# Optimization experiments

Hardware: AMD Instinct MI355X
Metric: run time of the kernel (lower is better)

The kernel has to match this reference:

```python
import jax, jax.numpy as jnp
import numpy as np

D = 1024      # in_dim
HS = 64       # head_size
H = 16        # num_heads
B, S = 2, 2048


def setup_inputs() -> dict:
    key = jax.random.key(0)
    k1, k2, k3, k4, k5, k6 = jax.random.split(key, 6)
    scale = 1.0 / np.sqrt(D)
    x = jax.random.normal(k1, (B, S, D), dtype=jnp.float32)
    # Stacked per-head projection weights (torch Linear weight is [out,in];
    # random init so layout only needs to be consistent). query weight exists
    # in the torch module but is never used (source bug), so it is omitted.
    Wk = jax.random.normal(k2, (H, D, HS), dtype=jnp.float32) * scale
    Wv = jax.random.normal(k3, (H, D, HS), dtype=jnp.float32) * scale
    Wproj = jax.random.normal(k4, (H * HS, D), dtype=jnp.float32) * (1.0 / np.sqrt(H * HS))
    bproj = jax.random.normal(k5, (D,), dtype=jnp.float32) * 0.01
    return {"x": x, "Wk": Wk, "Wv": Wv, "Wproj": Wproj, "bproj": bproj}


def reference(x, Wk, Wv, Wproj, bproj):
    # Faithful to source: k = key(x); q = value(x); v = value(x)  (q == v, no softmax)
    k = jnp.einsum("bsd,hde->bhse", x, Wk)   # [B,H,S,HS]
    v = jnp.einsum("bsd,hde->bhse", x, Wv)   # [B,H,S,HS]
    q = v
    inv_sqrt = jnp.asarray(HS, x.dtype) ** -0.5
    wei = jnp.einsum("bhse,bhte->bhst", q, k) * inv_sqrt  # [B,H,S,S], unnormalized
    out = jnp.einsum("bhst,bhte->bhse", wei, v)            # [B,H,S,HS]
    # concat heads: [B,S,H*HS]
    out = jnp.transpose(out, (0, 2, 1, 3)).reshape(x.shape[0], x.shape[1], H * HS)
    return out @ Wproj + bproj  # [B,S,D]
```

## Files before the change

kernel.cpp:

```cpp
#include <hip/hip_runtime.h>

#define B_ 2
#define S_ 2048
#define D_ 1024
#define H_ 16
#define HS_ 64
#define HD_ 1024
#define SPLIT 16
#define BS_ (B_*S_)
#define BK_ 64
#define BKO_ 128

typedef __attribute__((ext_vector_type(8))) short short8_t;
typedef __attribute__((ext_vector_type(4))) float float4_t;

__device__ inline unsigned short f32_to_bf16(float f) {
  unsigned int u = __float_as_uint(f);
  u += 0x7FFF + ((u >> 16) & 1);
  return (unsigned short)(u >> 16);
}

__device__ inline void async_copy16(const void* g, void* lds) {
  __builtin_amdgcn_global_load_lds(
      (const __attribute__((address_space(1))) void*)g,
      (__attribute__((address_space(3))) void*)lds, 16, 0, 0);
}


__global__ __launch_bounds__(256) void prep_kernel(
    const float* __restrict__ x, const float* __restrict__ Wk,
    const float* __restrict__ Wv, unsigned short* __restrict__ xb,
    unsigned short* __restrict__ Wkvt) {
  const int blk = blockIdx.x;
  const int tid = threadIdx.x;
  __shared__ float lds[64][65];
  if (blk < 4096) {
    int idx = blk * 256 + tid;
    float4 v = ((const float4*)x)[idx];
    ushort4 o;
    o.x = f32_to_bf16(v.x); o.y = f32_to_bf16(v.y);
    o.z = f32_to_bf16(v.z); o.w = f32_to_bf16(v.w);
    ((ushort4*)xb)[idx] = o;
    return;
  }
  const int wblk = blk - 4096;
  const int h = wblk >> 4;
  const int d0 = (wblk & 15) * 64;
#pragma unroll
  for (int i = 0; i < 16; ++i) {
    int idx = tid + i * 256; int dd = idx >> 6, e = idx & 63;
    lds[e][dd] = Wk[((size_t)h * D_ + d0 + dd) * HS_ + e];
  }
  __syncthreads();
#pragma unroll
  for (int i = 0; i < 16; ++i) {
    int idx = tid + i * 256; int e = idx >> 6, dd = idx & 63;
    Wkvt[((size_t)h * 128 + e) * D_ + d0 + dd] = f32_to_bf16(lds[e][dd]);
  }
  __syncthreads();
#pragma unroll
  for (int i = 0; i < 16; ++i) {
    int idx = tid + i * 256; int dd = idx >> 6, e = idx & 63;
    lds[e][dd] = Wv[((size_t)h * D_ + d0 + dd) * HS_ + e];
  }
  __syncthreads();
#pragma unroll
  for (int i = 0; i < 16; ++i) {
    int idx = tid + i * 256; int e = idx >> 6, dd = idx & 63;
    Wkvt[((size_t)h * 128 + 64 + e) * D_ + d0 + dd] = f32_to_bf16(lds[e][dd]);
  }
}

__global__ __launch_bounds__(256, 4) void kv_mfma_kernel(
    const unsigned short* __restrict__ xb,
    const unsigned short* __restrict__ Wkvt,
    unsigned short* __restrict__ Kt,
    unsigned short* __restrict__ Vb,
    unsigned short* __restrict__ Vt) {
  const int blk = blockIdx.x;
  const int stile = blk & 31;
  const int ntile = blk >> 5;
  const int h = ntile >> 1, half = ntile & 1;
  const int s0 = stile * 128;
  const int tid = threadIdx.x;
  const int lane = tid & 63;
  const int wid = tid >> 6;
  const int quad = lane >> 4, l16 = lane & 15;
  const int srow8 = lane >> 3;
  const int csw = ((lane & 7) ^ srow8) * 8;
  const int xa = l16 & 7;

  __shared__ __align__(16) unsigned short As[128 * BK_];
  __shared__ __align__(16) unsigned short Bs[64 * BK_];

  float4_t acc[2][4];
  const float4_t fz = {0.f, 0.f, 0.f, 0.f};
#pragma unroll
  for (int i = 0; i < 2; ++i)
#pragma unroll
    for (int j = 0; j < 4; ++j) acc[i][j] = fz;

  const unsigned short* Brow = Wkvt + ((size_t)h * 128 + half * 64) * D_;
  for (int k0 = 0; k0 < D_; k0 += BK_) {
#pragma unroll
    for (int i = 0; i < 4; ++i) {
      int g = wid * 4 + i;
      int r = g * 8 + srow8;
      async_copy16(xb + (size_t)(s0 + r) * D_ + k0 + csw, As + g * 8 * BK_);
    }
#pragma unroll
    for (int i = 0; i < 2; ++i) {
      int g = wid * 2 + i;
      int r = g * 8 + srow8;
      async_copy16(Brow + (size_t)r * D_ + k0 + csw, Bs + g * 8 * BK_);
    }
    __syncthreads();
    short8_t a[2][2], b[4][2];
#pragma unroll
    for (int mi = 0; mi < 2; ++mi)
#pragma unroll
      for (int ks = 0; ks < 2; ++ks)
        a[mi][ks] = *(const short8_t*)(As + (wid * 32 + mi * 16 + l16) * BK_ +
                                       ((ks * 4 + quad) ^ xa) * 8);
#pragma unroll
    for (int ni = 0; ni < 4; ++ni)
#pragma unroll
      for (int ks = 0; ks < 2; ++ks)
        b[ni][ks] = *(const short8_t*)(Bs + (ni * 16 + l16) * BK_ +
                                       ((ks * 4 + quad) ^ xa) * 8);
#pragma unroll
    for (int ks = 0; ks < 2; ++ks)
#pragma unroll
      for (int mi = 0; mi < 2; ++mi)
#pragma unroll
        for (int ni = 0; ni < 4; ++ni)
          acc[mi][ni] = __builtin_amdgcn_mfma_f32_16x16x32_bf16(
              a[mi][ks], b[ni][ks], acc[mi][ni], 0, 0, 0);
    __syncthreads();
  }
#pragma unroll
  for (int mi = 0; mi < 2; ++mi)
#pragma unroll
    for (int ni = 0; ni < 4; ++ni) {
      int fr = h * 64 + ni * 16 + l16;
      int sc = s0 + wid * 32 + mi * 16 + quad * 4;
      ushort4 o;
      o.x = f32_to_bf16(acc[mi][ni][0]);
      o.y = f32_to_bf16(acc[mi][ni][1]);
      o.z = f32_to_bf16(acc[mi][ni][2]);
      o.w = f32_to_bf16(acc[mi][ni][3]);
      if (half == 0) {
        *(ushort4*)&Kt[(size_t)fr * BS_ + sc] = o;
      } else {
        *(ushort4*)&Vt[(size_t)fr * BS_ + sc] = o;
#pragma unroll
        for (int r = 0; r < 4; ++r)
          Vb[(size_t)(sc + r) * HD_ + fr] = ((const unsigned short*)&o)[r];
      }
    }
}

__global__ __launch_bounds__(64) void m_partial_kernel(
    const unsigned short* __restrict__ Kt, const unsigned short* __restrict__ Vt,
    float* __restrict__ Mpart) {
  const int blk = blockIdx.x;
  const int h = blk & 15;
  const int b = (blk >> 4) & 1;
  const int split = blk >> 5;
  const int lane = threadIdx.x;
  const int quad = lane >> 4, l16 = lane & 15;
  const int sBase = b * S_ + split * (S_ / SPLIT);

  const unsigned short* Krow = Kt + (size_t)h * 64 * BS_;
  const unsigned short* Vrow = Vt + (size_t)h * 64 * BS_;

  float4_t acc[4][4];
  const float4_t fz = {0.f, 0.f, 0.f, 0.f};
#pragma unroll
  for (int i = 0; i < 4; ++i)
#pragma unroll
    for (int j = 0; j < 4; ++j) acc[i][j] = fz;

  for (int sc = 0; sc < S_ / SPLIT; sc += 32) {
    short8_t a[4], bfr[4];
#pragma unroll
    for (int mi = 0; mi < 4; ++mi)
      a[mi] = *(const short8_t*)&Krow[(size_t)(mi * 16 + l16) * BS_ + sBase + sc + quad * 8];
#pragma unroll
    for (int ni = 0; ni < 4; ++ni)
      bfr[ni] = *(const short8_t*)&Vrow[(size_t)(ni * 16 + l16) * BS_ + sBase + sc + quad * 8];
#pragma unroll
    for (int mi = 0; mi < 4; ++mi)
#pragma unroll
      for (int ni = 0; ni < 4; ++ni)
        acc[mi][ni] = __builtin_amdgcn_mfma_f32_16x16x32_bf16(
            a[mi], bfr[ni], acc[mi][ni], 0, 0, 0);
  }
  float* dst = Mpart + (((size_t)split * B_ + b) * H_ + h) * 4096;
#pragma unroll
  for (int mi = 0; mi < 4; ++mi)
#pragma unroll
    for (int ni = 0; ni < 4; ++ni)
#pragma unroll
      for (int r = 0; r < 4; ++r)
        dst[(mi * 16 + quad * 4 + r) * 64 + ni * 16 + l16] = acc[mi][ni][r];
}

__global__ __launch_bounds__(256) void m_reduce_kernel(
    const float* __restrict__ Mpart, float* __restrict__ M) {
  const int gid = blockIdx.x * 256 + threadIdx.x;
  const int e0 = gid * 4;
  const int bh = e0 >> 12;
  const int idx = e0 & 4095;
  float4 s = {0.f, 0.f, 0.f, 0.f};
#pragma unroll
  for (int p = 0; p < SPLIT; ++p) {
    const float4 v = *(const float4*)&Mpart[((size_t)(p * B_ * H_) + bh) * 4096 + idx];
    s.x += v.x; s.y += v.y; s.z += v.z; s.w += v.w;
  }
  s.x *= 0.125f; s.y *= 0.125f; s.z *= 0.125f; s.w *= 0.125f;
  *(float4*)&M[(size_t)bh * 4096 + idx] = s;
}

__global__ __launch_bounds__(256) void p_kernel(
    const float* __restrict__ M, const float* __restrict__ Wproj,
    unsigned short* __restrict__ Pt) {
  const int blk = blockIdx.x;
  const int dtile = blk & 15;
  const int h = (blk >> 4) & 15;
  const int b = blk >> 8;
  const int d0 = dtile * 64;
  const int tid = threadIdx.x;
  const int tx = tid & 15, ty = tid >> 4;
  __shared__ float Ms[64][68];
  __shared__ float Ws[64][68];
  const size_t mbase = ((size_t)(b * H_ + h)) * HS_ * HS_;
#pragma unroll
  for (int i = 0; i < 16; ++i) {
    int idx = tid + i * 256;
    int f = idx >> 6, e = idx & 63;
    Ms[e][f] = M[mbase + idx];
    Ws[f][e] = Wproj[(size_t)(h * HS_ + f) * D_ + d0 + e];
  }
  __syncthreads();
  float acc[4][4] = {};
#pragma unroll
  for (int kk = 0; kk < 64; ++kk) {
    const float4 a4 = *(const float4*)&Ms[kk][ty * 4];
    const float4 b4 = *(const float4*)&Ws[kk][tx * 4];
    const float a[4] = {a4.x, a4.y, a4.z, a4.w};
    const float bb[4] = {b4.x, b4.y, b4.z, b4.w};
#pragma unroll
    for (int i = 0; i < 4; ++i)
#pragma unroll
      for (int j = 0; j < 4; ++j) acc[i][j] += a[i] * bb[j];
  }
  __syncthreads();
#pragma unroll
  for (int i = 0; i < 4; ++i)
#pragma unroll
    for (int j = 0; j < 4; ++j)
      Ms[tx * 4 + j][ty * 4 + i] = acc[i][j];
  __syncthreads();
  {
    int c = tid >> 2, ch = tid & 3;
    unsigned short* dst = Pt + ((size_t)(b * D_ + d0 + c)) * HD_ + h * 64 + ch * 16;
#pragma unroll
    for (int e = 0; e < 16; ++e) dst[e] = f32_to_bf16(Ms[c][ch * 16 + e]);
  }
}

__global__ __launch_bounds__(256) void out_mfma_kernel(
    const unsigned short* __restrict__ Vb,
    const unsigned short* __restrict__ Pt,
    const float* __restrict__ bproj,
    float* __restrict__ out) {
  const int blk = blockIdx.x;
  const int ntile = blk & 15;
  const int stile = blk >> 4;
  const int s0 = stile * 128;
  const int n0 = ntile * 64;
  const int b = s0 >> 11;
  const int tid = threadIdx.x;
  const int lane = tid & 63;
  const int wid = tid >> 6;
  const int wm = wid & 1, wn = wid >> 1;
  const int quad = lane >> 4, l16 = lane & 15;
  const int srow4 = lane >> 4;
  const int xa = l16 & 7;

  __shared__ __align__(16) unsigned short As[128 * BKO_];
  __shared__ __align__(16) unsigned short Bs[64 * BKO_];

  float4_t acc[4][2];
  const float4_t fz = {0.f, 0.f, 0.f, 0.f};
#pragma unroll
  for (int i = 0; i < 4; ++i)
#pragma unroll
    for (int j = 0; j < 2; ++j) acc[i][j] = fz;

  const unsigned short* Bpanel = Pt + (size_t)b * D_ * HD_;
  for (int k0 = 0; k0 < HD_; k0 += BKO_) {
#pragma unroll
    for (int i = 0; i < 8; ++i) {
      int g = wid * 8 + i;
      int r = g * 4 + srow4;
      int ch = (l16 ^ (r & 7)) * 8;
      async_copy16(Vb + (size_t)(s0 + r) * HD_ + k0 + ch, As + g * 4 * BKO_);
    }
#pragma unroll
    for (int i = 0; i < 4; ++i) {
      int g = wid * 4 + i;
      int r = g * 4 + srow4;
      int ch = (l16 ^ (r & 7)) * 8;
      async_copy16(Bpanel + (size_t)(n0 + r) * HD_ + k0 + ch, Bs + g * 4 * BKO_);
    }
    __syncthreads();
    short8_t a[4][4], bfr[2][4];
#pragma unroll
    for (int mi = 0; mi < 4; ++mi)
#pragma unroll
      for (int ks = 0; ks < 4; ++ks)
        a[mi][ks] = *(const short8_t*)(As + (wm * 64 + mi * 16 + l16) * BKO_ +
                                       ((ks * 4 + quad) ^ xa) * 8);
#pragma unroll
    for (int ni = 0; ni < 2; ++ni)
#pragma unroll
      for (int ks = 0; ks < 4; ++ks)
        bfr[ni][ks] = *(const short8_t*)(Bs + (wn * 32 + ni * 16 + l16) * BKO_ +
                                         ((ks * 4 + quad) ^ xa) * 8);
#pragma unroll
    for (int ks = 0; ks < 4; ++ks)
#pragma unroll
      for (int mi = 0; mi < 4; ++mi)
#pragma unroll
        for (int ni = 0; ni < 2; ++ni)
          acc[mi][ni] = __builtin_amdgcn_mfma_f32_16x16x32_bf16(
              a[mi][ks], bfr[ni][ks], acc[mi][ni], 0, 0, 0);
    __syncthreads();
  }
#pragma unroll
  for (int ni = 0; ni < 2; ++ni) {
    int col = n0 + wn * 32 + ni * 16 + l16;
    float bias = bproj[col];
#pragma unroll
    for (int mi = 0; mi < 4; ++mi) {
      int rowb = s0 + wm * 64 + mi * 16 + quad * 4;
#pragma unroll
      for (int r = 0; r < 4; ++r)
        out[(size_t)(rowb + r) * D_ + col] = acc[mi][ni][r] + bias;
    }
  }
}

extern "C" void kernel_launch(void* const* d_in, const int* in_sizes, int n_in,
                              void* d_out, int out_size, void* d_ws, size_t ws_size,
                              hipStream_t stream) {
  const float* x = (const float*)d_in[0];
  const float* Wk = (const float*)d_in[1];
  const float* Wv = (const float*)d_in[2];
  const float* Wproj = (const float*)d_in[3];
  const float* bproj = (const float*)d_in[4];
  float* out = (float*)d_out;

  char* ws = (char*)d_ws;
  unsigned short* xb = (unsigned short*)ws;
  unsigned short* Wkvt = xb + (size_t)BS_ * D_;
  unsigned short* Kt = Wkvt + (size_t)H_ * 128 * D_;
  unsigned short* Vb = Kt + (size_t)HD_ * BS_;
  unsigned short* Vt = Vb + (size_t)BS_ * HD_;
  float* Mpart = (float*)(Vt + (size_t)HD_ * BS_);
  float* M = Mpart + (size_t)SPLIT * B_ * H_ * HS_ * HS_;
  unsigned short* Pt = (unsigned short*)(M + (size_t)B_ * H_ * HS_ * HS_);

  prep_kernel<<<dim3(4096 + H_ * (D_ / 64)), dim3(256), 0, stream>>>(x, Wk, Wv, xb, Wkvt);
  kv_mfma_kernel<<<dim3(32 * 32), dim3(256), 0, stream>>>(xb, Wkvt, Kt, Vb, Vt);
  m_partial_kernel<<<dim3(SPLIT * B_ * H_), dim3(64), 0, stream>>>(Kt, Vt, Mpart);
  m_reduce_kernel<<<dim3(128), dim3(256), 0, stream>>>(Mpart, M);
  p_kernel<<<dim3(B_ * H_ * (D_ / 64)), dim3(256), 0, stream>>>(M, Wproj, Pt);
  out_mfma_kernel<<<dim3(32 * 16), dim3(256), 0, stream>>>(Vb, Pt, bproj, out);
}
```

Before: 139.5 us.

## Fuse per-tile K^T V partial products into the KV projection kernel

```diff
diff --git a/kernel.cpp b/kernel.cpp
--- a/kernel.cpp
+++ b/kernel.cpp
@@ -6,10 +6,10 @@
 #define H_ 16
 #define HS_ 64
 #define HD_ 1024
-#define SPLIT 16
 #define BS_ (B_*S_)
 #define BK_ 64
 #define BKO_ 128
+#define TP_ 136
 
 typedef __attribute__((ext_vector_type(8))) short short8_t;
 typedef __attribute__((ext_vector_type(4))) float float4_t;
@@ -71,139 +71,123 @@
   }
 }
 
-__global__ __launch_bounds__(256, 4) void kv_mfma_kernel(
+__global__ __launch_bounds__(256) void kv_mfma_kernel(
     const unsigned short* __restrict__ xb,
     const unsigned short* __restrict__ Wkvt,
-    unsigned short* __restrict__ Kt,
     unsigned short* __restrict__ Vb,
-    unsigned short* __restrict__ Vt) {
+    float* __restrict__ Mpart) {
   const int blk = blockIdx.x;
   const int stile = blk & 31;
-  const int ntile = blk >> 5;
-  const int h = ntile >> 1, half = ntile & 1;
+  const int h = blk >> 5;
   const int s0 = stile * 128;
   const int tid = threadIdx.x;
   const int lane = tid & 63;
   const int wid = tid >> 6;
+  const int wm = wid & 1, wn = wid >> 1;
   const int quad = lane >> 4, l16 = lane & 15;
   const int srow8 = lane >> 3;
   const int csw = ((lane & 7) ^ srow8) * 8;
   const int xa = l16 & 7;
 
-  __shared__ __align__(16) unsigned short As[128 * BK_];
-  __shared__ __align__(16) unsigned short Bs[64 * BK_];
-
-  float4_t acc[2][4];
+  __shared__ __align__(16) unsigned char smem[2 * 64 * TP_ * 2];
+  unsigned short* As  = (unsigned short*)smem;
+  unsigned short* Bs  = (unsigned short*)(smem + 128 * BK_ * 2);
+  unsigned short* Ktl = (unsigned short*)smem;
+  unsigned short* Vtl = (unsigned short*)(smem + 64 * TP_ * 2);
+
+  float4_t acc[4][4];
   const float4_t fz = {0.f, 0.f, 0.f, 0.f};
 #pragma unroll
-  for (int i = 0; i < 2; ++i)
+  for (int i = 0; i < 4; ++i)
 #pragma unroll
     for (int j = 0; j < 4; ++j) acc[i][j] = fz;
 
-  const unsigned short* Brow = Wkvt + ((size_t)h * 128 + half * 64) * D_;
   for (int k0 = 0; k0 < D_; k0 += BK_) {
 #pragma unroll
     for (int i = 0; i < 4; ++i) {
       int g = wid * 4 + i;
       int r = g * 8 + srow8;
       async_copy16(xb + (size_t)(s0 + r) * D_ + k0 + csw, As + g * 8 * BK_);
-    }
-#pragma unroll
-    for (int i = 0; i < 2; ++i) {
-      int g = wid * 2 + i;
-      int r = g * 8 + srow8;
-      async_copy16(Brow + (size_t)r * D_ + k0 + csw, Bs + g * 8 * BK_);
+      async_copy16(Wkvt + ((size_t)h * 128 + r) * D_ + k0 + csw, Bs + g * 8 * BK_);
     }
     __syncthreads();
-    short8_t a[2][2], b[4][2];
-#pragma unroll
-    for (int mi = 0; mi < 2; ++mi)
+    short8_t a[4][2], b[4][2];
+#pragma unroll
+    for (int mi = 0; mi < 4; ++mi)
 #pragma unroll
       for (int ks = 0; ks < 2; ++ks)
-        a[mi][ks] = *(const short8_t*)(As + (wid * 32 + mi * 16 + l16) * BK_ +
+        a[mi][ks] = *(const short8_t*)(As + (wm * 64 + mi * 16 + l16) * BK_ +
                                        ((ks * 4 + quad) ^ xa) * 8);
 #pragma unroll
     for (int ni = 0; ni < 4; ++ni)
 #pragma unroll
       for (int ks = 0; ks < 2; ++ks)
-        b[ni][ks] = *(const short8_t*)(Bs + (ni * 16 + l16) * BK_ +
+        b[ni][ks] = *(const short8_t*)(Bs + (wn * 64 + ni * 16 + l16) * BK_ +
                                        ((ks * 4 + quad) ^ xa) * 8);
 #pragma unroll
     for (int ks = 0; ks < 2; ++ks)
 #pragma unroll
-      for (int mi = 0; mi < 2; ++mi)
+      for (int mi = 0; mi < 4; ++mi)
 #pragma unroll
         for (int ni = 0; ni < 4; ++ni)
           acc[mi][ni] = __builtin_amdgcn_mfma_f32_16x16x32_bf16(
               a[mi][ks], b[ni][ks], acc[mi][ni], 0, 0, 0);
     __syncthreads();
   }
-#pragma unroll
-  for (int mi = 0; mi < 2; ++mi)
+
+  {
+    unsigned short* dstT = (wn == 0) ? Ktl : Vtl;
+#pragma unroll
+    for (int mi = 0; mi < 4; ++mi)
+#pragma unroll
+      for (int ni = 0; ni < 4; ++ni) {
+        int f = ni * 16 + l16;
+        int sm = wm * 64 + mi * 16 + quad * 4;
+        ushort4 o;
+        o.x = f32_to_bf16(acc[mi][ni][0]);
+        o.y = f32_to_bf16(acc[mi][ni][1]);
+        o.z = f32_to_bf16(acc[mi][ni][2]);
+        o.w = f32_to_bf16(acc[mi][ni][3]);
+        *(ushort4*)&dstT[f * TP_ + sm] = o;
+      }
+  }
+  __syncthreads();
+
+#pragma unroll
+  for (int u = 0; u < 4; ++u) {
+    int unit = tid + u * 256;
+    int s = unit & 127;
+    int ec = (unit >> 7) * 8;
+    union { unsigned short u16[8]; uint4 v; } t;
+#pragma unroll
+    for (int e = 0; e < 8; ++e) t.u16[e] = Vtl[(ec + e) * TP_ + s];
+    *(uint4*)&Vb[(size_t)(s0 + s) * HD_ + h * 64 + ec] = t.v;
+  }
+
+  {
+    float4_t macc[4];
+#pragma unroll
+    for (int ni = 0; ni < 4; ++ni) macc[ni] = fz;
+#pragma unroll
+    for (int ss = 0; ss < 4; ++ss) {
+      short8_t ka = *(const short8_t*)&Ktl[(wid * 16 + l16) * TP_ + ss * 32 + quad * 8];
+#pragma unroll
+      for (int ni = 0; ni < 4; ++ni) {
+        short8_t vv = *(const short8_t*)&Vtl[(ni * 16 + l16) * TP_ + ss * 32 + quad * 8];
+        macc[ni] = __builtin_amdgcn_mfma_f32_16x16x32_bf16(ka, vv, macc[ni], 0, 0, 0);
+      }
+    }
+    float* mdst = Mpart + ((size_t)stile * H_ + h) * 4096;
 #pragma unroll
     for (int ni = 0; ni < 4; ++ni) {
-      int fr = h * 64 + ni * 16 + l16;
-      int sc = s0 + wid * 32 + mi * 16 + quad * 4;
-      ushort4 o;
-      o.x = f32_to_bf16(acc[mi][ni][0]);
-      o.y = f32_to_bf16(acc[mi][ni][1]);
-      o.z = f32_to_bf16(acc[mi][ni][2]);
-      o.w = f32_to_bf16(acc[mi][ni][3]);
-      if (half == 0) {
-        *(ushort4*)&Kt[(size_t)fr * BS_ + sc] = o;
-      } else {
-        *(ushort4*)&Vt[(size_t)fr * BS_ + sc] = o;
-#pragma unroll
-        for (int r = 0; r < 4; ++r)
-          Vb[(size_t)(sc + r) * HD_ + fr] = ((const unsigned short*)&o)[r];
+      int e = ni * 16 + l16;
+#pragma unroll
+      for (int r = 0; r < 4; ++r) {
+        int f = wid * 16 + quad * 4 + r;
+        mdst[f * 64 + e] = macc[ni][r];
       }
     }
-}
-
-__global__ __launch_bounds__(64) void m_partial_kernel(
-    const unsigned short* __restrict__ Kt, const unsigned short* __restrict__ Vt,
-    float* __restrict__ Mpart) {
-  const int blk = blockIdx.x;
-  const int h = blk & 15;
-  const int b = (blk >> 4) & 1;
-  const int split = blk >> 5;
-  const int lane = threadIdx.x;
-  const int quad = lane >> 4, l16 = lane & 15;
-  const int sBase = b * S_ + split * (S_ / SPLIT);
-
-  const unsigned short* Krow = Kt + (size_t)h * 64 * BS_;
-  const unsigned short* Vrow = Vt + (size_t)h * 64 * BS_;
-
-  float4_t acc[4][4];
-  const float4_t fz = {0.f, 0.f, 0.f, 0.f};
-#pragma unroll
-  for (int i = 0; i < 4; ++i)
-#pragma unroll
-    for (int j = 0; j < 4; ++j) acc[i][j] = fz;
-
-  for (int sc = 0; sc < S_ / SPLIT; sc += 32) {
-    short8_t a[4], bfr[4];
-#pragma unroll
-    for (int mi = 0; mi < 4; ++mi)
-      a[mi] = *(const short8_t*)&Krow[(size_t)(mi * 16 + l16) * BS_ + sBase + sc + quad * 8];
-#pragma unroll
-    for (int ni = 0; ni < 4; ++ni)
-      bfr[ni] = *(const short8_t*)&Vrow[(size_t)(ni * 16 + l16) * BS_ + sBase + sc + quad * 8];
-#pragma unroll
-    for (int mi = 0; mi < 4; ++mi)
-#pragma unroll
-      for (int ni = 0; ni < 4; ++ni)
-        acc[mi][ni] = __builtin_amdgcn_mfma_f32_16x16x32_bf16(
-            a[mi], bfr[ni], acc[mi][ni], 0, 0, 0);
-  }
-  float* dst = Mpart + (((size_t)split * B_ + b) * H_ + h) * 4096;
-#pragma unroll
-  for (int mi = 0; mi < 4; ++mi)
-#pragma unroll
-    for (int ni = 0; ni < 4; ++ni)
-#pragma unroll
-      for (int r = 0; r < 4; ++r)
-        dst[(mi * 16 + quad * 4 + r) * 64 + ni * 16 + l16] = acc[mi][ni][r];
+  }
 }
 
 __global__ __launch_bounds__(256) void m_reduce_kernel(
@@ -212,10 +196,12 @@
   const int e0 = gid * 4;
   const int bh = e0 >> 12;
   const int idx = e0 & 4095;
+  const int b = bh >> 4, h = bh & 15;
   float4 s = {0.f, 0.f, 0.f, 0.f};
 #pragma unroll
-  for (int p = 0; p < SPLIT; ++p) {
-    const float4 v = *(const float4*)&Mpart[((size_t)(p * B_ * H_) + bh) * 4096 + idx];
+  for (int p = 0; p < 16; ++p) {
+    const float4 v =
+        *(const float4*)&Mpart[(((size_t)(b * 16 + p)) * H_ + h) * 4096 + idx];
     s.x += v.x; s.y += v.y; s.z += v.z; s.w += v.w;
   }
   s.x *= 0.125f; s.y *= 0.125f; s.z *= 0.125f; s.w *= 0.125f;
@@ -366,16 +352,13 @@
   char* ws = (char*)d_ws;
   unsigned short* xb = (unsigned short*)ws;
   unsigned short* Wkvt = xb + (size_t)BS_ * D_;
-  unsigned short* Kt = Wkvt + (size_t)H_ * 128 * D_;
-  unsigned short* Vb = Kt + (size_t)HD_ * BS_;
-  unsigned short* Vt = Vb + (size_t)BS_ * HD_;
-  float* Mpart = (float*)(Vt + (size_t)HD_ * BS_);
-  float* M = Mpart + (size_t)SPLIT * B_ * H_ * HS_ * HS_;
-  unsigned short* Pt = (unsigned short*)(M + (size_t)B_ * H_ * HS_ * HS_);
+  unsigned short* Vb = Wkvt + (size_t)H_ * 128 * D_;
+  float* Mpart = (float*)(Vb + (size_t)BS_ * HD_);
+  float* M = Mpart + (size_t)32 * H_ * 4096;
+  unsigned short* Pt = (unsigned short*)(M + (size_t)B_ * H_ * 4096);
 
   prep_kernel<<<dim3(4096 + H_ * (D_ / 64)), dim3(256), 0, stream>>>(x, Wk, Wv, xb, Wkvt);
-  kv_mfma_kernel<<<dim3(32 * 32), dim3(256), 0, stream>>>(xb, Wkvt, Kt, Vb, Vt);
-  m_partial_kernel<<<dim3(SPLIT * B_ * H_), dim3(64), 0, stream>>>(Kt, Vt, Mpart);
+  kv_mfma_kernel<<<dim3(32 * H_), dim3(256), 0, stream>>>(xb, Wkvt, Vb, Mpart);
   m_reduce_kernel<<<dim3(128), dim3(256), 0, stream>>>(Mpart, M);
   p_kernel<<<dim3(B_ * H_ * (D_ / 64)), dim3(256), 0, stream>>>(M, Wproj, Pt);
   out_mfma_kernel<<<dim3(32 * 16), dim3(256), 0, stream>>>(Vb, Pt, bproj, out);
```

Result: faster. 133.6 us (-4.3%).
